# Optimization experiments

Measured on AMD Instinct MI355X. Metric: run time of the kernel, lower is better.

Reference implementation:

```python
import jax, jax.numpy as jnp
from jax import lax
import numpy as np

N, C_IN, C_OUT, H, W, DS = 32, 16, 1, 128, 128, 5
NC = C_OUT * C_IN  # channels fed to DUBlock convs (= out_nc*nc_d[0])


def autocorr(x, ds):
    """x:(N,C,H,W) -> xtx_raw:(N,C,C,2ds-1,2ds-1).
    xtx_raw[n,i,j,u,v] = sum_{h,w} x[n,i,h,w] * xpad[n,j,u+h,v+w]  (zero pad ds-1),
    matching torch cal_xtx (sample-wise conv3d of x with itself)."""
    n, c, h, w = x.shape
    p = ds - 1
    xp = jnp.pad(x, ((0, 0), (0, 0), (p, p), (p, p)))
    rows = []
    for u in range(2 * ds - 1):
        cols = [jnp.einsum('nihw,njhw->nij', x,
                           lax.slice(xp, (0, 0, u, v), (n, c, u + h, v + w)))
                for v in range(2 * ds - 1)]
        rows.append(jnp.stack(cols, axis=-1))
    return jnp.stack(rows, axis=-2)  # (N,C,C,K,K), K=2ds-1


def crosscorr(x, y, ds):
    """x:(N,Ci,H,W), y:(N,Co,H,W) -> xty:(N,Co,Ci,ds,ds)  (torch cal_xty, pad=(ds-1)//2)."""
    n, c, h, w = x.shape
    p = (ds - 1) // 2
    xp = jnp.pad(x, ((0, 0), (0, 0), (p, p), (p, p)))
    rows = []
    for u in range(ds):
        cols = [jnp.einsum('nohw,njhw->noj', y,
                           lax.slice(xp, (0, 0, u, v), (n, c, u + h, v + w)))
                for v in range(ds)]
        rows.append(jnp.stack(cols, axis=-1))
    return jnp.stack(rows, axis=-2)  # (N,Co,Ci,ds,ds)


def assemble_Q(R, ds):
    """Block-Toeplitz assembly. Equivalent to torch's unfold + flip + index permutation:
    Q[n,(i,p,q),(j,oi,oj)] = R[n,i,j, ds-1+oi-p, ds-1+oj-q]."""
    n, c = R.shape[0], R.shape[1]
    r = jnp.arange(ds)
    idx = (ds - 1) + r[None, :] - r[:, None]  # idx[p,o] = ds-1+o-p in [0, 2ds-2]
    Q6 = R[:, :, :, idx[:, None, :, None], idx[None, :, None, :]]  # (N,i,j,p,q,oi,oj)
    return jnp.transpose(Q6, (0, 1, 3, 4, 2, 5, 6)).reshape(n, c * ds * ds, c * ds * ds)


def dsb(x, d, y, alpha, reg):
    """DSBlock: regularized normal equations + batched SPD solve.
    x:(N,Ci,H,W), d:(N,Co,Ci,ds,ds), y:(N,Co,H,W), alpha:(N,1,1,1), reg:(1,)"""
    n, ci, h, w = x.shape
    co, ds = d.shape[1], d.shape[-1]
    Q = assemble_Q(autocorr(x, ds), ds)                               # (N, ci*ds^2, ci*ds^2)
    P = crosscorr(x, y, ds).reshape(n, co, -1).transpose(0, 2, 1)      # (N, ci*ds^2, co)
    a = alpha.reshape(n, 1, 1) * (h * w) * reg / (ds * ds * ci)        # (N,1,1)
    m = Q.shape[1]
    Q = Q + a * jnp.eye(m, dtype=Q.dtype)
    P = P + a * d.reshape(n, co, -1).transpose(0, 2, 1)
    # torch uses cholesky + cholesky_solve on SPD Q; jnp.linalg.solve computes the
    # same solution (and its vjp matches the custom CholeskySolve backward for symmetric Q).
    D = jnp.linalg.solve(Q, P)                                         # (N, ci*ds^2, co)
    return D.reshape(n, ci, ds, ds, co).transpose(0, 4, 1, 2, 3)       # (N,Co,Ci,ds,ds)


def conv3x3(x, wgt, b):
    o = lax.conv_general_dilated(x, wgt, (1, 1), ((1, 1), (1, 1)),
                                 dimension_numbers=('NCHW', 'OIHW', 'NCHW'))
    return o + b[None, :, None, None]


def dblock_fwd(x1, x2, d, y1, y2, alpha, beta, reg,
               w1, b1, w2, b2, w3, b3, w4, b4, w5, b5, w6, b6):
    d = dsb(x1, d, y1, alpha, reg)
    d = dsb(x2, d, y2, alpha, reg)
    n, co, ci, ds = d.shape[0], d.shape[1], d.shape[2], d.shape[3]
    bmap = jnp.broadcast_to(1.0 / jnp.sqrt(beta), (n, 1, ds, ds))      # (1/beta.sqrt()).repeat
    h0 = jnp.concatenate([d.reshape(n, co * ci, ds, ds), bmap], axis=1)
    # DUBlock
    t = jax.nn.relu(conv3x3(jax.nn.relu(conv3x3(h0, w1, b1)), w2, b2))
    t = jax.nn.relu(conv3x3(jax.nn.relu(conv3x3(t, w3, b3)), w4, b4))
    t = conv3x3(jax.nn.relu(conv3x3(t, w5, b5)), w6, b6) + h0[:, :-1]
    return t.reshape(n, co, ci, ds, ds)


def setup_inputs() -> dict:
    key = jax.random.key(0)
    ks = jax.random.split(key, 24)
    inp = {
        'x1': jax.random.normal(ks[0], (N, C_IN, H, W), jnp.float32),
        'x2': jax.random.normal(ks[1], (N, C_IN, H, W), jnp.float32),
        'd': jax.random.normal(ks[2], (N, C_OUT, C_IN, DS, DS), jnp.float32),
        'y1': jax.random.normal(ks[3], (N, C_OUT, H, W), jnp.float32),
        'y2': jax.random.normal(ks[4], (N, C_OUT, H, W), jnp.float32),
        'alpha': jax.random.uniform(ks[5], (N, 1, 1, 1), jnp.float32),
        'beta': jax.random.uniform(ks[6], (N, 1, 1, 1), jnp.float32),
        'reg': jnp.ones((1,), jnp.float32),
    }
    cins = [NC + 1, NC, NC, NC, NC, NC]
    for i in range(6):
        inp['w%d' % (i + 1)] = 0.05 * jax.random.normal(ks[7 + i], (NC, cins[i], 3, 3), jnp.float32)
        inp['b%d' % (i + 1)] = jnp.zeros((NC,), jnp.float32)
    return inp


def reference(x1, x2, d, y1, y2, alpha, beta, reg,
              w1, b1, w2, b2, w3, b3, w4, b4, w5, b5, w6, b6):
    return dblock_fwd(x1, x2, d, y1, y2, alpha, beta, reg,
                      w1, b1, w2, b2, w3, b3, w4, b4, w5, b5, w6, b6)
```

## Files before the change

kernel.cpp:

```cpp
#include <hip/hip_runtime.h>
#include <hip/hip_bf16.h>

constexpr int NS   = 32;
constexpr int C    = 16;
constexpr int H    = 128;
constexpr int W    = 128;
constexpr int DS   = 5;
constexpr int M    = C * DS * DS;
constexpr int NLAG = 81;

typedef short short8 __attribute__((ext_vector_type(8)));
typedef float f32x4 __attribute__((ext_vector_type(4)));

constexpr int CH_U    = 152;
constexpr int SLOT_U  = 16 * CH_U;
constexpr int SLOT_B  = SLOT_U * 2;
constexpr int RING_B  = 16 * SLOT_B;
constexpr int CHK     = 19;
constexpr size_t XB_US_PER_IN = (size_t)NS * H * 16 * CH_U;

constexpr int WREP_F  = 6 * 144 * 20 + 6 * 16;
constexpr int WREP_CH = WREP_F * 4 / 16;

constexpr int PVP = 29;

__device__ __forceinline__ unsigned int pk_bf16(float a, float b) {
    union { __hip_bfloat162 h; unsigned int u; } cv;
    cv.h = __float22bfloat162_rn(make_float2(a, b));
    return cv.u;
}

__device__ __forceinline__ void gl_lds16(const void* g, void* l) {
    __builtin_amdgcn_global_load_lds(
        (const __attribute__((address_space(1))) unsigned int*)g,
        (__attribute__((address_space(3))) unsigned int*)l, 16, 0, 0);
}

__global__ __launch_bounds__(256, 1)
void prep_kernel(const float* __restrict__ x1, const float* __restrict__ x2,
                 const float* __restrict__ y1, const float* __restrict__ y2,
                 unsigned short* __restrict__ xb,
                 float* __restrict__ P1, float* __restrict__ P2,
                 const float* __restrict__ w1, const float* __restrict__ b1,
                 const float* __restrict__ w2, const float* __restrict__ b2,
                 const float* __restrict__ w3, const float* __restrict__ b3,
                 const float* __restrict__ w4, const float* __restrict__ b4,
                 const float* __restrict__ w5, const float* __restrict__ b5,
                 const float* __restrict__ w6, const float* __restrict__ b6,
                 float* __restrict__ wrep)
{
    const int b = blockIdx.x, tid = threadIdx.x;
    if (b < 1024) {
        const int n = b & 31, zi = (b >> 5) & 1, rg = b >> 6;
        const float* xn = (zi ? x2 : x1) + (size_t)n * C * H * W;
        uint4* dst = (uint4*)(xb + (size_t)zi * XB_US_PER_IN +
                              ((size_t)n * H) * SLOT_U);
        for (int f = tid; f < 8 * 16 * CHK; f += 256) {
            const int rc = f / CHK, g = f - rc * CHK;
            const int row = rg * 8 + (rc >> 4), ch = rc & 15;
            uint4 o = make_uint4(0u, 0u, 0u, 0u);
            if (g >= 1 && g <= 16) {
                const float4* s4 = (const float4*)(xn + ((size_t)ch * H + row) * W + (g - 1) * 8);
                float4 va = s4[0], vb = s4[1];
                o.x = pk_bf16(va.x, va.y); o.y = pk_bf16(va.z, va.w);
                o.z = pk_bf16(vb.x, vb.y); o.w = pk_bf16(vb.z, vb.w);
            }
            dst[((size_t)row * 16 + ch) * CHK + g] = o;
        }
        return;
    }
    if (b < 2048) {
        const int b2 = b - 1024;
        const int n = b2 & 31, j = (b2 >> 5) & 15, zi = b2 >> 9;
        const float* x = zi ? x2 : x1;
        const float* y = zi ? y2 : y1;
        float* P       = zi ? P2 : P1;

        const float* yn = y + (size_t)n * H * W;
        const float* xc = x + ((size_t)n * C + j) * H * W;

        const int wg = tid & 31, slab = tid >> 5;
        const int r0 = slab * 16;

        float acc[25];
#pragma unroll
        for (int l = 0; l < 25; ++l) acc[l] = 0.f;

        float4 yw[5];
#pragma unroll
        for (int u = 0; u < 5; ++u) {
            const int t = r0 + 1 - u;
            yw[u] = (t >= 0) ? *(const float4*)(yn + (size_t)t * W + wg * 4)
                             : make_float4(0.f, 0.f, 0.f, 0.f);
        }

#pragma unroll 4
        for (int rr = 0; rr < 16; ++rr) {
            const int r = r0 + rr;
#pragma unroll
            for (int u = 4; u >= 1; --u) yw[u] = yw[u - 1];
            const int tnew = r + 2;
            yw[0] = (tnew < H) ? *(const float4*)(yn + (size_t)tnew * W + wg * 4)
                               : make_float4(0.f, 0.f, 0.f, 0.f);

            const float* xr = xc + (size_t)r * W + wg * 4;
            float w12[12];
            float4 t4 = (wg > 0) ? *(const float4*)(xr - 4) : make_float4(0, 0, 0, 0);
            w12[0] = t4.x; w12[1] = t4.y; w12[2] = t4.z; w12[3] = t4.w;
            t4 = *(const float4*)(xr);
            w12[4] = t4.x; w12[5] = t4.y; w12[6] = t4.z; w12[7] = t4.w;
            t4 = (wg < 31) ? *(const float4*)(xr + 4) : make_float4(0, 0, 0, 0);
            w12[8] = t4.x; w12[9] = t4.y; w12[10] = t4.z; w12[11] = t4.w;

#pragma unroll
            for (int u = 0; u < 5; ++u) {
#pragma unroll
                for (int v = 0; v < 5; ++v)
                    acc[u * 5 + v] += yw[u].x * w12[2 + v] + yw[u].y * w12[3 + v] +
                                      yw[u].z * w12[4 + v] + yw[u].w * w12[5 + v];
            }
        }

        __shared__ float red[4][25];
        const int lane = tid & 63, wv = tid >> 6;
#pragma unroll
        for (int l = 0; l < 25; ++l) {
            float v = acc[l];
#pragma unroll
            for (int off = 32; off; off >>= 1) v += __shfl_down(v, off);
            if (lane == 0) red[wv][l] = v;
        }
        __syncthreads();
        if (tid < 25)
            P[((size_t)n * C + j) * 25 + tid] = red[0][tid] + red[1][tid] + red[2][tid] + red[3][tid];
        return;
    }
    const float* wsl[6] = {w1, w2, w3, w4, w5, w6};
    const float* bsl[6] = {b1, b2, b3, b4, b5, b6};
#pragma unroll
    for (int l = 0; l < 6; ++l) {
        const int cin = (l == 0) ? 17 : 16;
        const float* ws = wsl[l];
        for (int f = tid; f < 16 * cin * 9; f += 256) {
            const int o = f / (cin * 9);
            const int rm = f - o * cin * 9;
            const int ci = rm / 9, kk = rm - ci * 9;
            wrep[l * 2880 + (o * 9 + kk) * 20 + ci] = ws[f];
        }
        if (tid < 16) wrep[17280 + l * 16 + tid] = bsl[l][tid];
    }
}

template<int P0, int P1>
__device__ __forceinline__ void autocorr_body(const unsigned short* __restrict__ xn,
                                              float* __restrict__ Rn,
                                              char* sm, int tid)
{
    constexpr int U0 = P0 / 9;
    constexpr int U1 = (P1 - 1) / 9;
    constexpr int NB = U1 - U0 + 1;
    constexpr int NP = P1 - P0;
    constexpr int SLOT_Q = SLOT_B / 16;

    unsigned short* ring = (unsigned short*)sm;
    const int lane = tid & 63;
    const int wid  = tid >> 6;
    const int q    = lane >> 4;
    const int mi   = lane & 15;
    const int rh   = wid & 3;
    const int chh  = wid >> 2;

    f32x4 acc[NP];
#pragma unroll
    for (int l = 0; l < NP; ++l) acc[l] = (f32x4){0.f, 0.f, 0.f, 0.f};

    const char* gb = (const char*)xn;

    for (int f = tid; f < 4 * SLOT_Q; f += 512)
        ((uint4*)sm)[(12 + f / SLOT_Q) * SLOT_Q + (f % SLOT_Q)] = make_uint4(0, 0, 0, 0);
    for (int f = wid; f < 38; f += 8)
        gl_lds16(gb + (size_t)f * 1024 + lane * 16, sm + f * 1024);
    __syncthreads();

    for (int s = 0; s < H; s += 4) {
        if (s < H - 8) {
            const size_t gbase = (size_t)(s + 8) * SLOT_B;
            char* lbase = sm + ((s + 8) & 15) * SLOT_B;
            for (int f = wid; f < 19; f += 8)
                gl_lds16(gb + gbase + (size_t)f * 1024 + lane * 16, lbase + f * 1024);
        } else {
            for (int f = tid; f < 4 * SLOT_Q; f += 512)
                ((uint4*)sm)[(((s + 8 + f / SLOT_Q) & 15)) * SLOT_Q + (f % SLOT_Q)] = make_uint4(0, 0, 0, 0);
        }

        const int r = s + rh;
        const unsigned short* rowA = ring + (r & 15) * SLOT_U + mi * CH_U;
#pragma unroll
        for (int cc = 0; cc < 2; ++cc) {
            const int w0 = (chh * 2 + cc) * 32;
            const uint4* pa = (const uint4*)(rowA + w0 + 8 * q);
            uint4 A0 = pa[0], A1 = pa[1], A2 = pa[2];
            unsigned int d[12] = {A0.x, A0.y, A0.z, A0.w, A1.x, A1.y, A1.z, A1.w,
                                  A2.x, A2.y, A2.z, A2.w};
            short8 bf[NB];
#pragma unroll
            for (int u = U0; u <= U1; ++u)
                bf[u - U0] = *(const short8*)(ring + ((r + u - 4 + 16) & 15) * SLOT_U +
                                              mi * CH_U + 8 + w0 + 8 * q);
#pragma unroll
            for (int v = 0; v < 9; ++v) {
                const int off = 12 - v;
                const int q4  = off >> 1;
                union { unsigned int u4[4]; short8 s8; } af;
                if (off & 1) {
#pragma unroll
                    for (int k2 = 0; k2 < 4; ++k2)
                        af.u4[k2] = (d[q4 + k2] >> 16) | (d[q4 + k2 + 1] << 16);
                } else {
#pragma unroll
                    for (int k2 = 0; k2 < 4; ++k2) af.u4[k2] = d[q4 + k2];
                }
#pragma unroll
                for (int u = U0; u <= U1; ++u) {
                    if (u * 9 + v >= P0 && u * 9 + v < P1)
                        acc[u * 9 + v - P0] = __builtin_amdgcn_mfma_f32_16x16x32_bf16(
                            af.s8, bf[u - U0], acc[u * 9 + v - P0], 0, 0, 0);
                }
            }
        }
        __syncthreads();
    }

    float* sred = (float*)sm;
#pragma unroll
    for (int cb = 0; cb < NP; cb += 9) {
        const int nc = (NP - cb < 9) ? (NP - cb) : 9;
        __syncthreads();
#pragma unroll
        for (int pp = 0; pp < 9; ++pp) {
            if (pp < nc) {
#pragma unroll
                for (int rg = 0; rg < 4; ++rg)
                    sred[(pp * 8 + wid) * 256 + (q * 4 + rg) * 16 + mi] = acc[cb + pp][rg];
            }
        }
        __syncthreads();
        if (tid < 256) {
#pragma unroll
            for (int pp = 0; pp < 9; ++pp) {
                if (pp < nc) {
                    float ssum = 0.f;
#pragma unroll
                    for (int w8 = 0; w8 < 8; ++w8)
                        ssum += sred[(pp * 8 + w8) * 256 + tid];
                    Rn[(size_t)tid * NLAG + P0 + cb + pp] = ssum;
                }
            }
        }
    }
}

__global__ __launch_bounds__(512, 2)
void autocorr_mfma(const unsigned short* __restrict__ xb,
                   float* __restrict__ R1, float* __restrict__ R2)
{
    __shared__ __align__(16) char sm[RING_B];
    const int n = blockIdx.x, zi = blockIdx.y, ug = blockIdx.z;
    const unsigned short* xn = xb + (size_t)zi * XB_US_PER_IN + (size_t)n * H * SLOT_U;
    float* Rn = (zi ? R2 : R1) + (size_t)n * C * C * NLAG;
    switch (ug) {
        case 0:  autocorr_body< 0, 20>(xn, Rn, sm, threadIdx.x); break;
        case 1:  autocorr_body<20, 40>(xn, Rn, sm, threadIdx.x); break;
        case 2:  autocorr_body<40, 60>(xn, Rn, sm, threadIdx.x); break;
        default: autocorr_body<60, 81>(xn, Rn, sm, threadIdx.x); break;
    }
}

__device__ __forceinline__ float block_sum256(float v, float* red, int t)
{
#pragma unroll
    for (int off = 32; off; off >>= 1) v += __shfl_down(v, off);
    if ((t & 63) == 0) red[t >> 6] = v;
    __syncthreads();
    float s = red[0] + red[1] + red[2] + red[3];
    __syncthreads();
    return s;
}

__device__ __forceinline__ void cg_solve(const float (&Rreg)[81],
                                         float rhs0, float rhs1,
                                         int iters, float a, int t, bool has1,
                                         float* pv, float* ap, float* red,
                                         float& z0o, float& z1o)
{
    const int jj = t & 15;
    const int e1 = t + 256;
    float z0 = 0.f, z1 = 0.f;
    float r0 = rhs0, r1 = has1 ? rhs1 : 0.f;
    float p0 = r0, p1 = r1;
    pv[(t / 25) * PVP + (t % 25)] = p0;
    if (has1) pv[(e1 / 25) * PVP + (e1 % 25)] = p1;
    float rr = block_sum256(r0 * r0 + r1 * r1, red, t);

    for (int it = 0; it < iters; ++it) {
        float pld[25], acc[25];
        const float* pj = &pv[jj * PVP];
#pragma unroll
        for (int k = 0; k < 25; ++k) pld[k] = pj[k];
#pragma unroll
        for (int k = 0; k < 25; ++k) acc[k] = 0.f;
#pragma unroll
        for (int u = 0; u < 9; ++u) {
#pragma unroll
            for (int v = 0; v < 9; ++v) {
                const float Rv = Rreg[u * 9 + v];
#pragma unroll
                for (int c = 0; c < 5; ++c) {
                    if (c < u - 4 || c > u) continue;
                    const int aa = 4 + c - u;
#pragma unroll
                    for (int dd = 0; dd < 5; ++dd) {
                        if (dd < v - 4 || dd > v) continue;
                        const int bb = 4 + dd - v;
                        acc[aa * 5 + bb] += Rv * pld[c * 5 + dd];
                    }
                }
            }
        }
#pragma unroll
        for (int k = 0; k < 25; ++k) {
            float s2 = acc[k];
            s2 += __shfl_down(s2, 8, 16);
            s2 += __shfl_down(s2, 4, 16);
            s2 += __shfl_down(s2, 2, 16);
            s2 += __shfl_down(s2, 1, 16);
            acc[k] = s2;
        }
        if (jj == 0) {
#pragma unroll
            for (int k = 0; k < 25; ++k) ap[(t >> 4) * 25 + k] = acc[k];
        }
        __syncthreads();
        const float w0 = ap[t] + a * p0;
        const float w1 = has1 ? (ap[e1] + a * p1) : 0.f;
        const float pAp = block_sum256(p0 * w0 + p1 * w1, red, t);
        const float al  = (pAp > 1e-30f) ? rr / pAp : 0.f;
        z0 += al * p0; z1 += al * p1;
        if (it + 1 < iters) {
            r0 -= al * w0; r1 -= al * w1;
            const float rrn = block_sum256(r0 * r0 + r1 * r1, red, t);
            const float be  = (rr > 1e-30f) ? rrn / rr : 0.f;
            rr = rrn;
            p0 = r0 + be * p0; p1 = r1 + be * p1;
            pv[(t / 25) * PVP + (t % 25)] = p0;
            if (has1) pv[(e1 / 25) * PVP + (e1 % 25)] = p1;
            __syncthreads();
        }
    }
    z0o = z0; z1o = z1;
}

__device__ __forceinline__ float conv_one(const float* __restrict__ act,
                                          const float* __restrict__ wall,
                                          int l, int idx)
{
    const int o = idx / 25, pix = idx % 25, yy = pix / 5, xx = pix % 5;
    float s = wall[17280 + l * 16 + o];
#pragma unroll
    for (int ky = 0; ky < 3; ++ky) {
        const int iy = yy + ky - 1;
        if ((unsigned)iy >= 5u) continue;
#pragma unroll
        for (int kx = 0; kx < 3; ++kx) {
            const int ix = xx + kx - 1;
            if ((unsigned)ix >= 5u) continue;
            const float* ip = act + (iy * 5 + ix) * 20;
            const float* wp = wall + l * 2880 + (o * 9 + ky * 3 + kx) * 20;
            const float4 a0 = *(const float4*)(ip);
            const float4 a1 = *(const float4*)(ip + 4);
            const float4 a2 = *(const float4*)(ip + 8);
            const float4 a3 = *(const float4*)(ip + 12);
            const float4 q0 = *(const float4*)(wp);
            const float4 q1 = *(const float4*)(wp + 4);
            const float4 q2 = *(const float4*)(wp + 8);
            const float4 q3 = *(const float4*)(wp + 12);
            s += a0.x * q0.x + a0.y * q0.y + a0.z * q0.z + a0.w * q0.w
               + a1.x * q1.x + a1.y * q1.y + a1.z * q1.z + a1.w * q1.w
               + a2.x * q2.x + a2.y * q2.y + a2.z * q2.z + a2.w * q2.w
               + a3.x * q3.x + a3.y * q3.y + a3.z * q3.z + a3.w * q3.w;
            if (l == 0) s += ip[16] * wp[16];
        }
    }
    return s;
}

__global__ __launch_bounds__(256, 1)
void solve_kernel(const float* __restrict__ R1, const float* __restrict__ R2,
                  const float* __restrict__ P1, const float* __restrict__ P2,
                  const float* __restrict__ d0, const float* __restrict__ alpha,
                  const float* __restrict__ beta, const float* __restrict__ reg,
                  const float* __restrict__ wrep,
                  float* __restrict__ out)
{
    __shared__ __align__(16) float Rl[256 * NLAG];
    __shared__ float pv[16 * PVP];
    __shared__ float ap[M];
    __shared__ float red[8];
    __shared__ float h0p[25 * 20];
    __shared__ float bufA[25 * 20], bufB[25 * 20];

    const int n = blockIdx.x, t = threadIdx.x;
    const bool has1 = (t < M - 256);
    const int e1 = t + 256;
    const float a = alpha[n] * (float)(H * W) * reg[0] / (float)(DS * DS * C);

    {
        const char* g = (const char*)(R1 + (size_t)n * 256 * NLAG);
        char* l = (char*)Rl;
        for (int f = t; f < 5184; f += 256)
            gl_lds16(g + (size_t)f * 16, l + (size_t)f * 16);
    }
    const float rhs10 = P1[(size_t)n * M + t] + a * d0[(size_t)n * M + t];
    const float rhs11 = has1 ? (P1[(size_t)n * M + e1] + a * d0[(size_t)n * M + e1]) : 0.f;
    __syncthreads();

    float Rreg[81];
    {
        const float* Rrow = &Rl[t * NLAG];
#pragma unroll
        for (int i = 0; i < 81; ++i) Rreg[i] = Rrow[i];
    }
    __syncthreads();

    {
        const char* g = (const char*)(R2 + (size_t)n * 256 * NLAG);
        char* l = (char*)Rl;
        for (int f = t; f < 5184; f += 256)
            gl_lds16(g + (size_t)f * 16, l + (size_t)f * 16);
    }
    float z1a, z1b;
    cg_solve(Rreg, rhs10, rhs11, 3, a, t, has1, pv, ap, red, z1a, z1b);
    {
        const float* Rrow = &Rl[t * NLAG];
#pragma unroll
        for (int i = 0; i < 81; ++i) Rreg[i] = Rrow[i];
    }
    __syncthreads();

    {
        const char* g = (const char*)wrep;
        char* l = (char*)Rl;
        for (int f = t; f < WREP_CH; f += 256)
            gl_lds16(g + (size_t)f * 16, l + (size_t)f * 16);
    }
    const float rhs20 = P2[(size_t)n * M + t] + a * z1a;
    const float rhs21 = has1 ? (P2[(size_t)n * M + e1] + a * z1b) : 0.f;
    float z20, z21;
    cg_solve(Rreg, rhs20, rhs21, 7, a, t, has1, pv, ap, red, z20, z21);

    const float* wall = (const float*)Rl;
    h0p[(t % 25) * 20 + t / 25] = z20;
    if (has1) h0p[(e1 % 25) * 20 + e1 / 25] = z21;
    if (t < 25) h0p[t * 20 + 16] = rsqrtf(beta[n]);
    __syncthreads();

#pragma unroll
    for (int l = 0; l < 6; ++l) {
        const float* act = (l == 0) ? h0p : ((l & 1) ? bufA : bufB);
        float s0 = conv_one(act, wall, l, t);
        float s1 = has1 ? conv_one(act, wall, l, e1) : 0.f;
        if (l < 5) { s0 = fmaxf(s0, 0.f); s1 = fmaxf(s1, 0.f); }
        else {
            s0 += h0p[(t % 25) * 20 + t / 25];
            if (has1) s1 += h0p[(e1 % 25) * 20 + e1 / 25];
        }
        if (l == 5) {
            out[(size_t)n * M + t] = s0;
            if (has1) out[(size_t)n * M + e1] = s1;
        } else {
            float* dstb = (l & 1) ? bufB : bufA;
            dstb[(t % 25) * 20 + t / 25] = s0;
            if (has1) dstb[(e1 % 25) * 20 + e1 / 25] = s1;
        }
        __syncthreads();
    }
}

extern "C" void kernel_launch(void* const* d_in, const int* in_sizes, int n_in,
                              void* d_out, int out_size, void* d_ws, size_t ws_size,
                              hipStream_t stream)
{
    (void)in_sizes; (void)n_in; (void)out_size; (void)ws_size;
    const float* x1    = (const float*)d_in[0];
    const float* x2    = (const float*)d_in[1];
    const float* d0    = (const float*)d_in[2];
    const float* y1    = (const float*)d_in[3];
    const float* y2    = (const float*)d_in[4];
    const float* alpha = (const float*)d_in[5];
    const float* beta  = (const float*)d_in[6];
    const float* reg   = (const float*)d_in[7];
    const float* w1 = (const float*)d_in[8];  const float* b1 = (const float*)d_in[9];
    const float* w2 = (const float*)d_in[10]; const float* b2 = (const float*)d_in[11];
    const float* w3 = (const float*)d_in[12]; const float* b3 = (const float*)d_in[13];
    const float* w4 = (const float*)d_in[14]; const float* b4 = (const float*)d_in[15];
    const float* w5 = (const float*)d_in[16]; const float* b5 = (const float*)d_in[17];
    const float* w6 = (const float*)d_in[18]; const float* b6 = (const float*)d_in[19];
    float* out = (float*)d_out;

    char* wsb = (char*)d_ws;
    unsigned short* xb = (unsigned short*)wsb;
    float* R1 = (float*)(wsb + 2 * XB_US_PER_IN * 2);
    const size_t RSZ = (size_t)NS * C * C * NLAG;
    float* R2 = R1 + RSZ;
    float* P1 = R2 + RSZ;
    float* P2 = P1 + (size_t)NS * M;
    float* wrep = P2 + (size_t)NS * M;

    prep_kernel<<<2049, 256, 0, stream>>>(x1, x2, y1, y2, xb, P1, P2,
                                          w1, b1, w2, b2, w3, b3, w4, b4,
                                          w5, b5, w6, b6, wrep);
    autocorr_mfma<<<dim3(NS, 2, 4), 512, 0, stream>>>(xb, R1, R2);
    solve_kernel<<<NS, 256, 0, stream>>>(R1, R2, P1, P2, d0, alpha, beta, reg,
                                         wrep, out);
}
```

Before: 263.5 us.

## Fuse bf16 conversion of x into autocorr kernel and remap blocks per XCD

Removes the prep stage that converted x1/x2 to a padded bf16 buffer in workspace. The autocorrelation kernel now loads fp32 rows directly, converts them to bf16 and writes them into the LDS ring, zeroing the pad columns itself. The grid becomes 1D, with a mapping that places the four lag-group blocks of the same sample on the same XCD so they can share L2. This saves a global write and read of the bf16 copy and one set of prep blocks. In exchange, each of the four lag-group blocks reads and converts the fp32 input separately, and the loads are now synchronous register loads rather than async global-to-LDS transfers.

```diff
diff --git a/kernel.cpp b/kernel.cpp
--- a/kernel.cpp
+++ b/kernel.cpp
@@ -16,8 +16,6 @@
 constexpr int SLOT_U  = 16 * CH_U;
 constexpr int SLOT_B  = SLOT_U * 2;
 constexpr int RING_B  = 16 * SLOT_B;
-constexpr int CHK     = 19;
-constexpr size_t XB_US_PER_IN = (size_t)NS * H * 16 * CH_U;
 
 constexpr int WREP_F  = 6 * 144 * 20 + 6 * 16;
 constexpr int WREP_CH = WREP_F * 4 / 16;
@@ -39,7 +37,6 @@
 __global__ __launch_bounds__(256, 1)
 void prep_kernel(const float* __restrict__ x1, const float* __restrict__ x2,
                  const float* __restrict__ y1, const float* __restrict__ y2,
-                 unsigned short* __restrict__ xb,
                  float* __restrict__ P1, float* __restrict__ P2,
                  const float* __restrict__ w1, const float* __restrict__ b1,
                  const float* __restrict__ w2, const float* __restrict__ b2,
@@ -51,27 +48,7 @@
 {
     const int b = blockIdx.x, tid = threadIdx.x;
     if (b < 1024) {
-        const int n = b & 31, zi = (b >> 5) & 1, rg = b >> 6;
-        const float* xn = (zi ? x2 : x1) + (size_t)n * C * H * W;
-        uint4* dst = (uint4*)(xb + (size_t)zi * XB_US_PER_IN +
-                              ((size_t)n * H) * SLOT_U);
-        for (int f = tid; f < 8 * 16 * CHK; f += 256) {
-            const int rc = f / CHK, g = f - rc * CHK;
-            const int row = rg * 8 + (rc >> 4), ch = rc & 15;
-            uint4 o = make_uint4(0u, 0u, 0u, 0u);
-            if (g >= 1 && g <= 16) {
-                const float4* s4 = (const float4*)(xn + ((size_t)ch * H + row) * W + (g - 1) * 8);
-                float4 va = s4[0], vb = s4[1];
-                o.x = pk_bf16(va.x, va.y); o.y = pk_bf16(va.z, va.w);
-                o.z = pk_bf16(vb.x, vb.y); o.w = pk_bf16(vb.z, vb.w);
-            }
-            dst[((size_t)row * 16 + ch) * CHK + g] = o;
-        }
-        return;
-    }
-    if (b < 2048) {
-        const int b2 = b - 1024;
-        const int n = b2 & 31, j = (b2 >> 5) & 15, zi = b2 >> 9;
+        const int n = b & 31, j = (b >> 5) & 15, zi = b >> 9;
         const float* x = zi ? x2 : x1;
         const float* y = zi ? y2 : y1;
         float* P       = zi ? P2 : P1;
@@ -151,8 +128,25 @@
     }
 }
 
+__device__ __forceinline__ void stage4(const float* __restrict__ xn,
+                                       char* sm, int row0, int tid)
+{
+    const int pair = tid >> 3;
+    const int sub  = tid & 7;
+    const int rr   = pair >> 4;
+    const int ch   = pair & 15;
+    const int row  = row0 + rr;
+    const float4* src = (const float4*)(xn + ((size_t)ch * H + row) * W + sub * 16);
+    const float4 a = src[0], b = src[1], c = src[2], d = src[3];
+    unsigned short* dst = (unsigned short*)sm + (row & 15) * SLOT_U + ch * CH_U + 8 + sub * 16;
+    *(uint4*)(dst)     = make_uint4(pk_bf16(a.x, a.y), pk_bf16(a.z, a.w),
+                                    pk_bf16(b.x, b.y), pk_bf16(b.z, b.w));
+    *(uint4*)(dst + 8) = make_uint4(pk_bf16(c.x, c.y), pk_bf16(c.z, c.w),
+                                    pk_bf16(d.x, d.y), pk_bf16(d.z, d.w));
+}
+
 template<int P0, int P1>
-__device__ __forceinline__ void autocorr_body(const unsigned short* __restrict__ xn,
+__device__ __forceinline__ void autocorr_body(const float* __restrict__ xn,
                                               float* __restrict__ Rn,
                                               char* sm, int tid)
 {
@@ -174,20 +168,22 @@
 #pragma unroll
     for (int l = 0; l < NP; ++l) acc[l] = (f32x4){0.f, 0.f, 0.f, 0.f};
 
-    const char* gb = (const char*)xn;
-
     for (int f = tid; f < 4 * SLOT_Q; f += 512)
         ((uint4*)sm)[(12 + f / SLOT_Q) * SLOT_Q + (f % SLOT_Q)] = make_uint4(0, 0, 0, 0);
-    for (int f = wid; f < 38; f += 8)
-        gl_lds16(gb + (size_t)f * 1024 + lane * 16, sm + f * 1024);
+    if (tid < 192) {
+        const int slot = tid >> 4, ch = tid & 15;
+        unsigned short* sb = ring + slot * SLOT_U + ch * CH_U;
+        *(uint4*)(sb)       = make_uint4(0u, 0u, 0u, 0u);
+        *(uint4*)(sb + 136) = make_uint4(0u, 0u, 0u, 0u);
+        *(uint4*)(sb + 144) = make_uint4(0u, 0u, 0u, 0u);
+    }
+    stage4(xn, sm, 0, tid);
+    stage4(xn, sm, 4, tid);
     __syncthreads();
 
     for (int s = 0; s < H; s += 4) {
         if (s < H - 8) {
-            const size_t gbase = (size_t)(s + 8) * SLOT_B;
-            char* lbase = sm + ((s + 8) & 15) * SLOT_B;
-            for (int f = wid; f < 19; f += 8)
-                gl_lds16(gb + gbase + (size_t)f * 1024 + lane * 16, lbase + f * 1024);
+            stage4(xn, sm, s + 8, tid);
         } else {
             for (int f = tid; f < 4 * SLOT_Q; f += 512)
                 ((uint4*)sm)[(((s + 8 + f / SLOT_Q) & 15)) * SLOT_Q + (f % SLOT_Q)] = make_uint4(0, 0, 0, 0);
@@ -261,12 +257,16 @@
 }
 
 __global__ __launch_bounds__(512, 2)
-void autocorr_mfma(const unsigned short* __restrict__ xb,
+void autocorr_mfma(const float* __restrict__ x1, const float* __restrict__ x2,
                    float* __restrict__ R1, float* __restrict__ R2)
 {
     __shared__ __align__(16) char sm[RING_B];
-    const int n = blockIdx.x, zi = blockIdx.y, ug = blockIdx.z;
-    const unsigned short* xn = xb + (size_t)zi * XB_US_PER_IN + (size_t)n * H * SLOT_U;
+    const int b = blockIdx.x;
+    const int xcd = b & 7, k = b >> 3;
+    const int slice = xcd * 8 + (k >> 2);
+    const int ug = k & 3;
+    const int n = slice & 31, zi = slice >> 5;
+    const float* xn = (zi ? x2 : x1) + (size_t)n * C * H * W;
     float* Rn = (zi ? R2 : R1) + (size_t)n * C * C * NLAG;
     switch (ug) {
         case 0:  autocorr_body< 0, 20>(xn, Rn, sm, threadIdx.x); break;
@@ -508,18 +508,17 @@
     float* out = (float*)d_out;
 
     char* wsb = (char*)d_ws;
-    unsigned short* xb = (unsigned short*)wsb;
-    float* R1 = (float*)(wsb + 2 * XB_US_PER_IN * 2);
+    float* R1 = (float*)wsb;
     const size_t RSZ = (size_t)NS * C * C * NLAG;
     float* R2 = R1 + RSZ;
     float* P1 = R2 + RSZ;
     float* P2 = P1 + (size_t)NS * M;
     float* wrep = P2 + (size_t)NS * M;
 
-    prep_kernel<<<2049, 256, 0, stream>>>(x1, x2, y1, y2, xb, P1, P2,
+    prep_kernel<<<1025, 256, 0, stream>>>(x1, x2, y1, y2, P1, P2,
                                           w1, b1, w2, b2, w3, b3, w4, b4,
                                           w5, b5, w6, b6, wrep);
-    autocorr_mfma<<<dim3(NS, 2, 4), 512, 0, stream>>>(xb, R1, R2);
+    autocorr_mfma<<<256, 512, 0, stream>>>(x1, x2, R1, R2);
     solve_kernel<<<NS, 256, 0, stream>>>(R1, R2, P1, P2, d0, alpha, beta, reg,
                                          wrep, out);
 }
```

Result: faster. 256.0 us (-2.9%).
